# Kernel tuning notes

Measured on AMD Instinct MI355X. Metric: run time of the kernel, lower is better.

The kernel has to match this reference:

```python
import jax, jax.numpy as jnp
import numpy as np

N_NODES = 50000


def setup_inputs() -> dict:
    key = jax.random.key(0)
    k1, k2, k3 = jax.random.split(key, 3)
    B, E, HS = 4, 800000, 16
    H = jax.random.normal(k1, (B, N_NODES, HS, HS), dtype=jnp.float32)
    edge_index = jax.random.randint(k2, (B, E, 2), 0, N_NODES, dtype=jnp.int32)
    edge_weight = jax.random.normal(k3, (B, E), dtype=jnp.float32)
    node_idx = jnp.arange(N_NODES, dtype=jnp.int32)  # identity id->row map
    return {"H": H, "edge_index": edge_index, "edge_weight": edge_weight,
            "node_idx": node_idx}


def reference(H, edge_index, edge_weight, node_idx):
    # Original builds adj[b, node1, node2] = w, krons with eye(h_size), and does
    # sparse.mm(H_adj, H). Blockwise this is exactly:
    #   out[b, u, :, :] = sum_{edges (u, v) in batch b} w * H[b, v, :, :]
    # node_idx maps raw node ids to rows; with arange it is the identity, so we
    # index by id directly (faithful to torch.where(node_idx == id)).
    inv = jnp.argsort(node_idx)  # id -> row (identity for arange)

    def agg_one(Hb, eb, wb):
        src_rows = inv[eb[:, 1]]  # node2: gathered neighbor
        dst_rows = inv[eb[:, 0]]  # node1: aggregation target
        msgs = Hb[src_rows] * wb[:, None, None]  # (E, hs, hs)
        return jax.ops.segment_sum(msgs, dst_rows, num_segments=N_NODES)

    return jax.vmap(agg_one)(H, edge_index, edge_weight)
```

## Files before the change

kernel.cpp:

```cpp
#include <hip/hip_runtime.h>


constexpr int ROW = 256;

typedef _Float16 half4 __attribute__((ext_vector_type(4)));
typedef float fvec4 __attribute__((ext_vector_type(4)));

static __device__ inline float h2f_bits(unsigned short u) {
    _Float16 h; __builtin_memcpy(&h, &u, 2); return (float)h;
}

__global__ void k_init(const int* __restrict__ nidx, int* __restrict__ inv,
                       int* __restrict__ zbuf, int nz, int N) {
    int i = blockIdx.x * blockDim.x + threadIdx.x;
    if (i < N) inv[nidx[i]] = i;
    if (i < nz) zbuf[i] = 0;
}

__global__ __launch_bounds__(256)
void k_prep(const fvec4* __restrict__ H, half4* __restrict__ Hh, size_t n4, int cvtBlocks,
            int scatBlocks,
            const unsigned long long* __restrict__ ei, const float* __restrict__ ew,
            const int* __restrict__ inv, int* __restrict__ cursor,
            unsigned* __restrict__ edges, int B, int E, int N, int cap) {
    if ((int)blockIdx.x < cvtBlocks) {
        size_t stride = (size_t)cvtBlocks * 256;
        for (size_t i = (size_t)blockIdx.x * 256 + threadIdx.x; i < n4; i += stride) {
            fvec4 v = __builtin_nontemporal_load(&H[i]);
            half4 o;
            o.x = (_Float16)v.x; o.y = (_Float16)v.y;
            o.z = (_Float16)v.z; o.w = (_Float16)v.w;
            Hh[i] = o;
        }
    } else {
        int total = B * E;
        int stride = scatBlocks * 256;
        for (int idx = ((int)blockIdx.x - cvtBlocks) * 256 + (int)threadIdx.x;
             idx < total; idx += stride) {
            unsigned long long pq = __builtin_nontemporal_load(&ei[idx]);
            int b = idx / E;
            int dst = inv[(int)(pq & 0xFFFFFFFFull)];
            int src = inv[(int)(pq >> 32)];
            float w = __builtin_nontemporal_load(&ew[idx]);
            _Float16 hw = (_Float16)w;
            unsigned short wb; __builtin_memcpy(&wb, &hw, 2);
            unsigned rec = (unsigned)(unsigned short)src | ((unsigned)wb << 16);
            int pos = atomicAdd(&cursor[(size_t)b * N + dst], 1);
            if (pos < cap)
                __builtin_nontemporal_store(rec, &edges[((size_t)b * N + dst) * cap + pos]);
        }
    }
}

__device__ inline void fma4(fvec4& acc, float w, half4 h) {
    acc.x += w * (float)h.x; acc.y += w * (float)h.y;
    acc.z += w * (float)h.z; acc.w += w * (float)h.w;
}

__global__ __launch_bounds__(256)
void k_agg_gap(const _Float16* __restrict__ Hh, const int* __restrict__ cursor,
               const unsigned* __restrict__ edges, float* __restrict__ out,
               int B, int N, int cap, int xpb) {
    int lane = threadIdx.x & 63;
    int wid = threadIdx.x >> 6;
    int b, grp;
    if (xpb > 0) {
        int bi = blockIdx.x;
        int xcd = bi & 7;
        b = xcd / xpb;
        grp = (bi >> 3) * xpb + (xcd % xpb);
    } else {
        b = blockIdx.y;
        grp = blockIdx.x;
    }
    int node = grp * 4 + wid;
    if (node >= N) return;
    int deg = cursor[(size_t)b * N + node];
    if (deg > cap) deg = cap;
    const unsigned* seg = edges + ((size_t)b * N + node) * cap;
    unsigned rec = 0;
    if (lane < deg) rec = __builtin_nontemporal_load(&seg[lane]);
    const half4* Hb = (const half4*)(Hh + (size_t)b * N * ROW);
    fvec4 acc = {0.f, 0.f, 0.f, 0.f};
    int j = 0;
    for (; j + 8 <= deg; j += 8) {
        int sv[8]; float wv[8];
#pragma unroll
        for (int u = 0; u < 8; ++u) {
            unsigned r = __shfl(rec, j + u);
            sv[u] = (int)(r & 0xFFFFu);
            wv[u] = h2f_bits((unsigned short)(r >> 16));
        }
        half4 hv[8];
#pragma unroll
        for (int u = 0; u < 8; ++u) hv[u] = Hb[(size_t)sv[u] * 64 + lane];
#pragma unroll
        for (int u = 0; u < 8; ++u) fma4(acc, wv[u], hv[u]);
    }
    if (j + 4 <= deg) {
        int sv[4]; float wv[4];
#pragma unroll
        for (int u = 0; u < 4; ++u) {
            unsigned r = __shfl(rec, j + u);
            sv[u] = (int)(r & 0xFFFFu);
            wv[u] = h2f_bits((unsigned short)(r >> 16));
        }
        half4 hv[4];
#pragma unroll
        for (int u = 0; u < 4; ++u) hv[u] = Hb[(size_t)sv[u] * 64 + lane];
#pragma unroll
        for (int u = 0; u < 4; ++u) fma4(acc, wv[u], hv[u]);
        j += 4;
    }
    for (; j < deg; ++j) {
        unsigned r = __shfl(rec, j);
        half4 h = Hb[(size_t)(r & 0xFFFFu) * 64 + lane];
        fma4(acc, h2f_bits((unsigned short)(r >> 16)), h);
    }
    __builtin_nontemporal_store(acc, (fvec4*)out + ((size_t)b * N + node) * 64 + lane);
}

__global__ void k_zero_f32(float* __restrict__ p, size_t n) {
    size_t i = (size_t)blockIdx.x * blockDim.x + threadIdx.x;
    if (i < n) p[i] = 0.f;
}

__global__ void k_atomic_agg(const float* __restrict__ H, const int* __restrict__ ei,
                             const float* __restrict__ ew, const int* __restrict__ inv,
                             float* __restrict__ out, int B, int E, int N) {
    int lane = threadIdx.x & 63;
    int widx = (blockIdx.x * blockDim.x + threadIdx.x) >> 6;
    int total = B * E;
    if (widx >= total) return;
    int b = widx / E;
    int d = ei[(size_t)widx * 2];
    int s = ei[(size_t)widx * 2 + 1];
    if (inv) { d = inv[d]; s = inv[s]; }
    float w = ew[widx];
    const float4* hp = (const float4*)(H + ((size_t)b * N + s) * ROW);
    float4 h = hp[lane];
    float* op = out + ((size_t)b * N + d) * ROW + lane * 4;
    atomicAdd(op + 0, w * h.x);
    atomicAdd(op + 1, w * h.y);
    atomicAdd(op + 2, w * h.z);
    atomicAdd(op + 3, w * h.w);
}

extern "C" void kernel_launch(void* const* d_in, const int* in_sizes, int n_in,
                              void* d_out, int out_size, void* d_ws, size_t ws_size,
                              hipStream_t stream) {
    const float* H = (const float*)d_in[0];
    const int* ei = (const int*)d_in[1];
    const float* ew = (const float*)d_in[2];
    const int* nidx = (const int*)d_in[3];
    float* out = (float*)d_out;

    int N = in_sizes[3];
    int B = in_sizes[0] / (N * ROW);
    int E = in_sizes[2] / B;
    int total = B * E;
    size_t nH = (size_t)B * N * ROW;

    char* w0 = (char*)d_ws;
    int* g_inv = (int*)w0;
    int* g_cursor = g_inv + N;
    size_t eoff = (((size_t)(N + (size_t)B * N) * 4) + 255) & ~(size_t)255;
    unsigned* g_edges = (unsigned*)(w0 + eoff);
    int cap = 0;
    size_t hoff = 0;
    for (int c : {64, 48}) {
        size_t ho = (eoff + (size_t)B * N * c * 4 + 255) & ~(size_t)255;
        if (ws_size >= ho + nH * 2) { cap = c; hoff = ho; break; }
    }

    if (cap > 0 && N <= 65535) {
        _Float16* Hh = (_Float16*)(w0 + hoff);
        int nz = B * N;
        int ninit = max(N, nz);
        k_init<<<(ninit + 255) / 256, 256, 0, stream>>>(nidx, g_inv, g_cursor, nz, N);
        int cvtBlocks = 1280;
        int scatBlocks = 768;
        k_prep<<<cvtBlocks + scatBlocks, 256, 0, stream>>>(
            (const fvec4*)H, (half4*)Hh, nH / 4, cvtBlocks, scatBlocks,
            (const unsigned long long*)ei, ew, g_inv, g_cursor, g_edges, B, E, N, cap);

        int groupsPerB = (N + 3) / 4;
        int xpb = (B > 0 && 8 % B == 0) ? 8 / B : 0;
        bool can_swz = xpb > 0 && (groupsPerB % xpb) == 0 &&
                       (((size_t)groupsPerB * B) % 8) == 0;
        if (can_swz) {
            k_agg_gap<<<groupsPerB * B, 256, 0, stream>>>(
                Hh, g_cursor, g_edges, out, B, N, cap, xpb);
        } else {
            dim3 ag(groupsPerB, B);
            k_agg_gap<<<ag, 256, 0, stream>>>(Hh, g_cursor, g_edges, out, B, N, cap, 0);
        }
        return;
    }

    int* finv = nullptr;
    if (ws_size >= (size_t)N * sizeof(int)) {
        finv = (int*)d_ws;
        k_init<<<(N + 255) / 256, 256, 0, stream>>>(nidx, finv, finv, 0, N);
    }
    size_t on = (size_t)out_size;
    k_zero_f32<<<(int)((on + 255) / 256), 256, 0, stream>>>(out, on);
    int blocks = (total * 64 + 255) / 256;
    k_atomic_agg<<<blocks, 256, 0, stream>>>(H, ei, ew, finv, out, B, E, N);
}
```

Measured before the change: 406.9 us.

## Bin edges by source tile and aggregate tile-by-tile with overflow atomics

Replaces the per-destination edge lists with bins split into 8 source-node tiles of 6 slots each. Edges that do not fit go to an overflow list, which a final kernel adds into the output with atomics. Aggregation walks the tiles in order, with a block barrier between tiles, so gathers of H rows stay in a narrower source range and should hit cache more often. The FP16 convert and the edge scatter now run as separate kernels instead of sharing one fused launch. In exchange the gather loop loses its 8-wide unrolled batched loads, gains barriers, zeroes a larger cursor array, and silently drops edges if the overflow list exceeds its fixed capacity.

```diff
diff --git a/kernel.cpp b/kernel.cpp
--- a/kernel.cpp
+++ b/kernel.cpp
@@ -2,6 +2,10 @@
 
 
 constexpr int ROW = 256;
+constexpr int TILES = 8;
+constexpr int BCAP = 6;
+constexpr int SLOTS = TILES * BCAP;
+constexpr int OVFCAP = 262144;
 
 typedef _Float16 half4 __attribute__((ext_vector_type(4)));
 typedef float fvec4 __attribute__((ext_vector_type(4)));
@@ -15,6 +19,121 @@
     int i = blockIdx.x * blockDim.x + threadIdx.x;
     if (i < N) inv[nidx[i]] = i;
     if (i < nz) zbuf[i] = 0;
+}
+
+__global__ __launch_bounds__(256)
+void k_cvt(const fvec4* __restrict__ H, half4* __restrict__ Hh, size_t n4) {
+    size_t stride = (size_t)gridDim.x * 256;
+    for (size_t i = (size_t)blockIdx.x * 256 + threadIdx.x; i < n4; i += stride) {
+        fvec4 v = __builtin_nontemporal_load(&H[i]);
+        half4 o;
+        o.x = (_Float16)v.x; o.y = (_Float16)v.y;
+        o.z = (_Float16)v.z; o.w = (_Float16)v.w;
+        Hh[i] = o;
+    }
+}
+
+__global__ __launch_bounds__(256)
+void k_scat(const unsigned long long* __restrict__ ei, const float* __restrict__ ew,
+            const int* __restrict__ inv, int* __restrict__ cursor,
+            unsigned* __restrict__ bins, int* __restrict__ ovfcnt,
+            uint2* __restrict__ ovf, int B, int E, int N, int tileSz) {
+    int total = B * E;
+    int stride = gridDim.x * 256;
+    for (int idx = blockIdx.x * 256 + (int)threadIdx.x; idx < total; idx += stride) {
+        unsigned long long pq = __builtin_nontemporal_load(&ei[idx]);
+        int b = idx / E;
+        int dst = inv[(int)(pq & 0xFFFFFFFFull)];
+        int src = inv[(int)(pq >> 32)];
+        float w = __builtin_nontemporal_load(&ew[idx]);
+        _Float16 hw = (_Float16)w;
+        unsigned short wb; __builtin_memcpy(&wb, &hw, 2);
+        unsigned rec = (unsigned)(unsigned short)src | ((unsigned)wb << 16);
+        int tile = src / tileSz;
+        size_t cidx = (size_t)(b * N + dst) * TILES + tile;
+        int pos = atomicAdd(&cursor[cidx], 1);
+        if (pos < BCAP) {
+            __builtin_nontemporal_store(rec, &bins[cidx * BCAP + pos]);
+        } else {
+            int op = atomicAdd(ovfcnt, 1);
+            if (op < OVFCAP)
+                ovf[op] = make_uint2(((unsigned)b << 16) | (unsigned)dst, rec | ((unsigned)0));
+        }
+    }
+}
+
+__device__ inline void fma4(fvec4& acc, float w, half4 h) {
+    acc.x += w * (float)h.x; acc.y += w * (float)h.y;
+    acc.z += w * (float)h.z; acc.w += w * (float)h.w;
+}
+
+__global__ __launch_bounds__(256)
+void k_agg_tiled(const _Float16* __restrict__ Hh, const int* __restrict__ cursor,
+                 const unsigned* __restrict__ bins, float* __restrict__ out,
+                 int B, int N, int xpb) {
+    int lane = threadIdx.x & 63;
+    int wid = threadIdx.x >> 6;
+    int b, grp;
+    if (xpb > 0) {
+        int bi = blockIdx.x;
+        int xcd = bi & 7;
+        b = xcd / xpb;
+        grp = (bi >> 3) * xpb + (xcd % xpb);
+    } else {
+        b = blockIdx.y;
+        grp = blockIdx.x;
+    }
+    int node = grp * 4 + wid;
+    bool valid = node < N;
+    int nn = valid ? node : 0;
+
+    unsigned rec = 0;
+    int cv = 0;
+    const unsigned* seg = bins + (size_t)(b * N + nn) * SLOTS;
+    if (lane < SLOTS) rec = __builtin_nontemporal_load(&seg[lane]);
+    if (lane >= SLOTS && lane < SLOTS + TILES)
+        cv = cursor[(size_t)(b * N + nn) * TILES + (lane - SLOTS)];
+
+    const half4* Hb = (const half4*)(Hh + (size_t)b * N * ROW);
+    fvec4 acc = {0.f, 0.f, 0.f, 0.f};
+#pragma unroll
+    for (int t = 0; t < TILES; ++t) {
+        if (t) __syncthreads();
+        int cnt = __shfl(cv, SLOTS + t);
+        if (cnt > BCAP) cnt = BCAP;
+        if (valid) {
+            for (int j = 0; j < cnt; ++j) {
+                unsigned r = __shfl(rec, t * BCAP + j);
+                half4 h = Hb[(size_t)(r & 0xFFFFu) * 64 + lane];
+                fma4(acc, h2f_bits((unsigned short)(r >> 16)), h);
+            }
+        }
+    }
+    if (valid)
+        __builtin_nontemporal_store(acc, (fvec4*)out + ((size_t)b * N + node) * 64 + lane);
+}
+
+__global__ __launch_bounds__(256)
+void k_ovf(const _Float16* __restrict__ Hh, const int* __restrict__ ovfcnt,
+           const uint2* __restrict__ ovf, float* __restrict__ out, int N) {
+    int lane = threadIdx.x & 63;
+    int wv = (blockIdx.x * 256 + (int)threadIdx.x) >> 6;
+    int nw = gridDim.x * 4;
+    int count = *ovfcnt;
+    if (count > OVFCAP) count = OVFCAP;
+    for (int i = wv; i < count; i += nw) {
+        uint2 v = ovf[i];
+        int b = (int)(v.x >> 16);
+        int dst = (int)(v.x & 0xFFFFu);
+        int src = (int)(v.y & 0xFFFFu);
+        float w = h2f_bits((unsigned short)(v.y >> 16));
+        half4 h = ((const half4*)(Hh + (size_t)b * N * ROW))[(size_t)src * 64 + lane];
+        float* op = out + ((size_t)b * N + dst) * ROW + lane * 4;
+        atomicAdd(op + 0, w * (float)h.x);
+        atomicAdd(op + 1, w * (float)h.y);
+        atomicAdd(op + 2, w * (float)h.z);
+        atomicAdd(op + 3, w * (float)h.w);
+    }
 }
 
 __global__ __launch_bounds__(256)
@@ -50,11 +169,6 @@
                 __builtin_nontemporal_store(rec, &edges[((size_t)b * N + dst) * cap + pos]);
         }
     }
-}
-
-__device__ inline void fma4(fvec4& acc, float w, half4 h) {
-    acc.x += w * (float)h.x; acc.y += w * (float)h.y;
-    acc.z += w * (float)h.z; acc.w += w * (float)h.w;
 }
 
 __global__ __launch_bounds__(256)
@@ -96,21 +210,6 @@
         for (int u = 0; u < 8; ++u) hv[u] = Hb[(size_t)sv[u] * 64 + lane];
 #pragma unroll
         for (int u = 0; u < 8; ++u) fma4(acc, wv[u], hv[u]);
-    }
-    if (j + 4 <= deg) {
-        int sv[4]; float wv[4];
-#pragma unroll
-        for (int u = 0; u < 4; ++u) {
-            unsigned r = __shfl(rec, j + u);
-            sv[u] = (int)(r & 0xFFFFu);
-            wv[u] = h2f_bits((unsigned short)(r >> 16));
-        }
-        half4 hv[4];
-#pragma unroll
-        for (int u = 0; u < 4; ++u) hv[u] = Hb[(size_t)sv[u] * 64 + lane];
-#pragma unroll
-        for (int u = 0; u < 4; ++u) fma4(acc, wv[u], hv[u]);
-        j += 4;
     }
     for (; j < deg; ++j) {
         unsigned r = __shfl(rec, j);
@@ -146,6 +245,8 @@
     atomicAdd(op + 3, w * h.w);
 }
 
+static inline size_t alignup(size_t x) { return (x + 255) & ~(size_t)255; }
+
 extern "C" void kernel_launch(void* const* d_in, const int* in_sizes, int n_in,
                               void* d_out, int out_size, void* d_ws, size_t ws_size,
                               hipStream_t stream) {
@@ -160,30 +261,64 @@
     int E = in_sizes[2] / B;
     int total = B * E;
     size_t nH = (size_t)B * N * ROW;
-
     char* w0 = (char*)d_ws;
+
+    size_t o_inv = 0;
+    size_t o_cur = alignup(o_inv + (size_t)N * 4);
+    size_t nz = (size_t)B * N * TILES + 1;
+    size_t o_ovf = alignup(o_cur + nz * 4);
+    size_t o_bins = alignup(o_ovf + (size_t)OVFCAP * 8);
+    size_t o_hh = alignup(o_bins + (size_t)B * N * SLOTS * 4);
+    size_t req_tiled = o_hh + nH * 2;
+
+    if (ws_size >= req_tiled && N <= 65535 && B <= 65535) {
+        int* t_inv = (int*)(w0 + o_inv);
+        int* t_cur = (int*)(w0 + o_cur);
+        int* t_ovfcnt = t_cur + (size_t)B * N * TILES;
+        uint2* t_ovf = (uint2*)(w0 + o_ovf);
+        unsigned* t_bins = (unsigned*)(w0 + o_bins);
+        _Float16* Hh = (_Float16*)(w0 + o_hh);
+        int tileSz = (N + TILES - 1) / TILES;
+
+        int ninit = max((size_t)N, nz);
+        k_init<<<(ninit + 255) / 256, 256, 0, stream>>>(nidx, t_inv, t_cur, (int)nz, N);
+        k_cvt<<<2048, 256, 0, stream>>>((const fvec4*)H, (half4*)Hh, nH / 4);
+        k_scat<<<2048, 256, 0, stream>>>((const unsigned long long*)ei, ew, t_inv,
+                                         t_cur, t_bins, t_ovfcnt, t_ovf, B, E, N, tileSz);
+        int groupsPerB = (N + 3) / 4;
+        int xpb = (B > 0 && 8 % B == 0) ? 8 / B : 0;
+        bool can_swz = xpb > 0 && (groupsPerB % xpb) == 0 &&
+                       (((size_t)groupsPerB * B) % 8) == 0;
+        if (can_swz) {
+            k_agg_tiled<<<groupsPerB * B, 256, 0, stream>>>(Hh, t_cur, t_bins, out, B, N, xpb);
+        } else {
+            dim3 ag(groupsPerB, B);
+            k_agg_tiled<<<ag, 256, 0, stream>>>(Hh, t_cur, t_bins, out, B, N, 0);
+        }
+        k_ovf<<<256, 256, 0, stream>>>(Hh, t_ovfcnt, t_ovf, out, N);
+        return;
+    }
+
     int* g_inv = (int*)w0;
     int* g_cursor = g_inv + N;
-    size_t eoff = (((size_t)(N + (size_t)B * N) * 4) + 255) & ~(size_t)255;
+    size_t eoff = alignup((size_t)(N + (size_t)B * N) * 4);
     unsigned* g_edges = (unsigned*)(w0 + eoff);
     int cap = 0;
     size_t hoff = 0;
     for (int c : {64, 48}) {
-        size_t ho = (eoff + (size_t)B * N * c * 4 + 255) & ~(size_t)255;
+        size_t ho = alignup(eoff + (size_t)B * N * c * 4);
         if (ws_size >= ho + nH * 2) { cap = c; hoff = ho; break; }
     }
 
     if (cap > 0 && N <= 65535) {
         _Float16* Hh = (_Float16*)(w0 + hoff);
-        int nz = B * N;
-        int ninit = max(N, nz);
-        k_init<<<(ninit + 255) / 256, 256, 0, stream>>>(nidx, g_inv, g_cursor, nz, N);
-        int cvtBlocks = 1280;
-        int scatBlocks = 768;
+        int nzg = B * N;
+        int ninit = max(N, nzg);
+        k_init<<<(ninit + 255) / 256, 256, 0, stream>>>(nidx, g_inv, g_cursor, nzg, N);
+        int cvtBlocks = 1280, scatBlocks = 768;
         k_prep<<<cvtBlocks + scatBlocks, 256, 0, stream>>>(
             (const fvec4*)H, (half4*)Hh, nH / 4, cvtBlocks, scatBlocks,
             (const unsigned long long*)ei, ew, g_inv, g_cursor, g_edges, B, E, N, cap);
-
         int groupsPerB = (N + 3) / 4;
         int xpb = (B > 0 && 8 % B == 0) ? 8 / B : 0;
         bool can_swz = xpb > 0 && (groupsPerB % xpb) == 0 &&
```

Result: slower. 598.6 us (+47.1%).

## Shrink per-node edge bucket to 32 and add overflow list with atomic pass

Applied to the files above, without the earlier changes.

The per-node edge bucket capacity drops from 64/48 to a fixed 32 slots. Edges beyond that go to a global overflow list, which a new kernel applies with float atomics after the main gather-aggregation. This cuts the bucket footprint and the scatter write traffic, and makes overflow edges correct where the old code silently dropped them. The split between conversion and scatter blocks is also rebalanced toward scatter. The extra launch and any atomic contention on the overflow path are the cost.

```diff
diff --git a/kernel.cpp b/kernel.cpp
--- a/kernel.cpp
+++ b/kernel.cpp
@@ -2,6 +2,8 @@
 
 
 constexpr int ROW = 256;
+constexpr int CAP = 32;
+constexpr int OVFCAP = 262144;
 
 typedef _Float16 half4 __attribute__((ext_vector_type(4)));
 typedef float fvec4 __attribute__((ext_vector_type(4)));
@@ -22,7 +24,8 @@
             int scatBlocks,
             const unsigned long long* __restrict__ ei, const float* __restrict__ ew,
             const int* __restrict__ inv, int* __restrict__ cursor,
-            unsigned* __restrict__ edges, int B, int E, int N, int cap) {
+            unsigned* __restrict__ edges, int* __restrict__ ovfcnt,
+            uint2* __restrict__ ovf, int B, int E, int N) {
     if ((int)blockIdx.x < cvtBlocks) {
         size_t stride = (size_t)cvtBlocks * 256;
         for (size_t i = (size_t)blockIdx.x * 256 + threadIdx.x; i < n4; i += stride) {
@@ -45,9 +48,15 @@
             _Float16 hw = (_Float16)w;
             unsigned short wb; __builtin_memcpy(&wb, &hw, 2);
             unsigned rec = (unsigned)(unsigned short)src | ((unsigned)wb << 16);
-            int pos = atomicAdd(&cursor[(size_t)b * N + dst], 1);
-            if (pos < cap)
-                __builtin_nontemporal_store(rec, &edges[((size_t)b * N + dst) * cap + pos]);
+            size_t sidx = (size_t)b * N + dst;
+            int pos = atomicAdd(&cursor[sidx], 1);
+            if (pos < CAP) {
+                __builtin_nontemporal_store(rec, &edges[sidx * CAP + pos]);
+            } else {
+                int op = atomicAdd(ovfcnt, 1);
+                if (op < OVFCAP)
+                    ovf[op] = make_uint2(((unsigned)b << 16) | (unsigned)dst, rec);
+            }
         }
     }
 }
@@ -60,7 +69,7 @@
 __global__ __launch_bounds__(256)
 void k_agg_gap(const _Float16* __restrict__ Hh, const int* __restrict__ cursor,
                const unsigned* __restrict__ edges, float* __restrict__ out,
-               int B, int N, int cap, int xpb) {
+               int B, int N, int xpb) {
     int lane = threadIdx.x & 63;
     int wid = threadIdx.x >> 6;
     int b, grp;
@@ -75,9 +84,10 @@
     }
     int node = grp * 4 + wid;
     if (node >= N) return;
-    int deg = cursor[(size_t)b * N + node];
-    if (deg > cap) deg = cap;
-    const unsigned* seg = edges + ((size_t)b * N + node) * cap;
+    size_t sidx = (size_t)b * N + node;
+    int deg = cursor[sidx];
+    if (deg > CAP) deg = CAP;
+    const unsigned* seg = edges + sidx * CAP;
     unsigned rec = 0;
     if (lane < deg) rec = __builtin_nontemporal_load(&seg[lane]);
     const half4* Hb = (const half4*)(Hh + (size_t)b * N * ROW);
@@ -117,7 +127,30 @@
         half4 h = Hb[(size_t)(r & 0xFFFFu) * 64 + lane];
         fma4(acc, h2f_bits((unsigned short)(r >> 16)), h);
     }
-    __builtin_nontemporal_store(acc, (fvec4*)out + ((size_t)b * N + node) * 64 + lane);
+    __builtin_nontemporal_store(acc, (fvec4*)out + (sidx * 64 + lane));
+}
+
+__global__ __launch_bounds__(256)
+void k_ovf(const _Float16* __restrict__ Hh, const int* __restrict__ ovfcnt,
+           const uint2* __restrict__ ovf, float* __restrict__ out, int N) {
+    int lane = threadIdx.x & 63;
+    int wv = (blockIdx.x * 256 + (int)threadIdx.x) >> 6;
+    int nw = gridDim.x * 4;
+    int count = *ovfcnt;
+    if (count > OVFCAP) count = OVFCAP;
+    for (int i = wv; i < count; i += nw) {
+        uint2 v = ovf[i];
+        int b = (int)(v.x >> 16);
+        int dst = (int)(v.x & 0xFFFFu);
+        int src = (int)(v.y & 0xFFFFu);
+        float w = h2f_bits((unsigned short)(v.y >> 16));
+        half4 h = ((const half4*)(Hh + (size_t)b * N * ROW))[(size_t)src * 64 + lane];
+        float* op = out + ((size_t)b * N + dst) * ROW + lane * 4;
+        atomicAdd(op + 0, w * (float)h.x);
+        atomicAdd(op + 1, w * (float)h.y);
+        atomicAdd(op + 2, w * (float)h.z);
+        atomicAdd(op + 3, w * (float)h.w);
+    }
 }
 
 __global__ void k_zero_f32(float* __restrict__ p, size_t n) {
@@ -146,6 +179,8 @@
     atomicAdd(op + 3, w * h.w);
 }
 
+static inline size_t alignup(size_t x) { return (x + 255) & ~(size_t)255; }
+
 extern "C" void kernel_launch(void* const* d_in, const int* in_sizes, int n_in,
                               void* d_out, int out_size, void* d_ws, size_t ws_size,
                               hipStream_t stream) {
@@ -160,29 +195,32 @@
     int E = in_sizes[2] / B;
     int total = B * E;
     size_t nH = (size_t)B * N * ROW;
-
     char* w0 = (char*)d_ws;
-    int* g_inv = (int*)w0;
-    int* g_cursor = g_inv + N;
-    size_t eoff = (((size_t)(N + (size_t)B * N) * 4) + 255) & ~(size_t)255;
-    unsigned* g_edges = (unsigned*)(w0 + eoff);
-    int cap = 0;
-    size_t hoff = 0;
-    for (int c : {64, 48}) {
-        size_t ho = (eoff + (size_t)B * N * c * 4 + 255) & ~(size_t)255;
-        if (ws_size >= ho + nH * 2) { cap = c; hoff = ho; break; }
-    }
-
-    if (cap > 0 && N <= 65535) {
-        _Float16* Hh = (_Float16*)(w0 + hoff);
-        int nz = B * N;
+
+    size_t o_inv = 0;
+    size_t o_cur = alignup(o_inv + (size_t)N * 4);
+    size_t ncur = (size_t)B * N + 1;
+    size_t o_ovf = alignup(o_cur + ncur * 4);
+    size_t o_seg = alignup(o_ovf + (size_t)OVFCAP * 8);
+    size_t o_hh = alignup(o_seg + (size_t)B * N * CAP * 4);
+    size_t req = o_hh + nH * 2;
+
+    if (ws_size >= req && N <= 65535 && B <= 65535) {
+        int* g_inv = (int*)(w0 + o_inv);
+        int* g_cursor = (int*)(w0 + o_cur);
+        int* g_ovfcnt = g_cursor + (size_t)B * N;
+        uint2* g_ovf = (uint2*)(w0 + o_ovf);
+        unsigned* g_edges = (unsigned*)(w0 + o_seg);
+        _Float16* Hh = (_Float16*)(w0 + o_hh);
+
+        int nz = (int)ncur;
         int ninit = max(N, nz);
         k_init<<<(ninit + 255) / 256, 256, 0, stream>>>(nidx, g_inv, g_cursor, nz, N);
-        int cvtBlocks = 1280;
-        int scatBlocks = 768;
+        int cvtBlocks = 896, scatBlocks = 1152;
         k_prep<<<cvtBlocks + scatBlocks, 256, 0, stream>>>(
             (const fvec4*)H, (half4*)Hh, nH / 4, cvtBlocks, scatBlocks,
-            (const unsigned long long*)ei, ew, g_inv, g_cursor, g_edges, B, E, N, cap);
+            (const unsigned long long*)ei, ew, g_inv, g_cursor, g_edges,
+            g_ovfcnt, g_ovf, B, E, N);
 
         int groupsPerB = (N + 3) / 4;
         int xpb = (B > 0 && 8 % B == 0) ? 8 / B : 0;
@@ -190,11 +228,12 @@
                        (((size_t)groupsPerB * B) % 8) == 0;
         if (can_swz) {
             k_agg_gap<<<groupsPerB * B, 256, 0, stream>>>(
-                Hh, g_cursor, g_edges, out, B, N, cap, xpb);
+                Hh, g_cursor, g_edges, out, B, N, xpb);
         } else {
             dim3 ag(groupsPerB, B);
-            k_agg_gap<<<ag, 256, 0, stream>>>(Hh, g_cursor, g_edges, out, B, N, cap, 0);
-        }
+            k_agg_gap<<<ag, 256, 0, stream>>>(Hh, g_cursor, g_edges, out, B, N, 0);
+        }
+        k_ovf<<<256, 256, 0, stream>>>(Hh, g_ovfcnt, g_ovf, out, N);
         return;
     }
 
```

Result: no change. 400.4 us (median of 2 runs) (-1.6%).
